# Kernel optimization log

Hardware: AMD Instinct MI355X
Metric: run time of the kernel (lower is better)

The kernel has to match this reference:

```python
import jax, jax.numpy as jnp
import numpy as np

B, S, E = 2, 2048, 1024
H = 16
D = E // H  # 64
SCALE = D ** -0.5


def setup_inputs() -> dict:
    key = jax.random.key(0)
    ks = jax.random.split(key, 9)
    w = lambda k: jax.random.normal(k, (E, E), dtype=jnp.float32) * 0.02
    b = lambda k: jax.random.normal(k, (E,), dtype=jnp.float32) * 0.02
    return {
        "hidden_states": jax.random.normal(ks[0], (B, S, E), dtype=jnp.float32),
        "q_w": w(ks[1]), "q_b": b(ks[2]),
        "k_w": w(ks[3]), "k_b": b(ks[4]),
        "v_w": w(ks[5]), "v_b": b(ks[6]),
        "o_w": w(ks[7]), "o_b": b(ks[8]),
    }


def reference(hidden_states, q_w, q_b, k_w, k_b, v_w, v_b, o_w, o_b):
    dtype = hidden_states.dtype
    # torch Linear: y = x @ W^T + b
    q = hidden_states @ q_w.T + q_b
    k = hidden_states @ k_w.T + k_b
    v = hidden_states @ v_w.T + v_b
    # [B,S,E] -> [B*H, S, D]
    split = lambda t: t.reshape(B, S, H, D).transpose(0, 2, 1, 3).reshape(B * H, S, D)
    q, k, v = split(q), split(k), split(v)
    # upcast_attention: fp32 QK^T, scaled (baddbmm with beta=0, no mask)
    scores = SCALE * jnp.einsum("bqd,bkd->bqk", q.astype(jnp.float32), k.astype(jnp.float32))
    # upcast_softmax: fp32 softmax over last dim (transpose_qk=False), cast back
    probs = jax.nn.softmax(scores, axis=-1).astype(dtype)
    # PV bmm, merge heads, out_proj (dropout p=0.0 -> identity)
    out = jnp.einsum("bqk,bkd->bqd", probs, v)
    out = out.reshape(B, H, S, D).transpose(0, 2, 1, 3).reshape(B, S, E)
    return out @ o_w.T + o_b
```

## Files before the change

kernel.cpp:

```cpp
#include <hip/hip_runtime.h>

typedef __bf16 bf16x8 __attribute__((ext_vector_type(8)));
typedef __bf16 bf16x4 __attribute__((ext_vector_type(4)));
typedef float  f32x4  __attribute__((ext_vector_type(4)));
typedef float  f32x16 __attribute__((ext_vector_type(16)));
typedef unsigned int u32x4 __attribute__((ext_vector_type(4)));

#define CS 0.18033688011112042f

__device__ __forceinline__ float fast_exp2(float x) {
    return __builtin_amdgcn_exp2f(x);
}

__device__ __forceinline__ f32x4 MFMA(bf16x8 a, bf16x8 b, f32x4 c) {
    return __builtin_amdgcn_mfma_f32_16x16x32_bf16(a, b, c, 0, 0, 0);
}
__device__ __forceinline__ f32x16 MFMA32(bf16x8 a, bf16x8 b, f32x16 c) {
    return __builtin_amdgcn_mfma_f32_32x32x16_bf16(a, b, c, 0, 0, 0);
}

__device__ __forceinline__ unsigned pk2(float a, float b) {
    union { __bf16 h[2]; unsigned u; } x;
    x.h[0] = (__bf16)a; x.h[1] = (__bf16)b;
    return x.u;
}

__device__ __forceinline__ void swap32(unsigned &a, unsigned &b) {
    asm volatile("v_permlane32_swap_b32 %0, %1" : "+v"(a), "+v"(b));
}

__global__ __launch_bounds__(256) void cvt5_kernel(
    const float* __restrict__ s0, const float* __restrict__ s1,
    const float* __restrict__ s2, const float* __restrict__ s3,
    const float* __restrict__ s4,
    __bf16* __restrict__ d0, __bf16* __restrict__ d1, __bf16* __restrict__ d2,
    __bf16* __restrict__ d3, __bf16* __restrict__ d4)
{
    int blk = blockIdx.x;
    const float* src; __bf16* dst; int base;
    if (blk < 4096)      { src = s0; dst = d0; base = blk; }
    else if (blk < 5120) { src = s1; dst = d1; base = blk - 4096; }
    else if (blk < 6144) { src = s2; dst = d2; base = blk - 5120; }
    else if (blk < 7168) { src = s3; dst = d3; base = blk - 6144; }
    else                 { src = s4; dst = d4; base = blk - 7168; }
    int i = base * 1024 + threadIdx.x * 4;
    float4 v = *(const float4*)(src + i);
    bf16x4 o;
    o[0] = (__bf16)v.x; o[1] = (__bf16)v.y; o[2] = (__bf16)v.z; o[3] = (__bf16)v.w;
    *(bf16x4*)(dst + i) = o;
}

template <typename OutT, int BN>
__device__ __forceinline__ void gemm_core(const __bf16* __restrict__ A,
                                          const __bf16* __restrict__ W,
                                          const float* __restrict__ bias,
                                          OutT* __restrict__ C,
                                          int m0, int n0, bool vtrans)
{
    constexpr int NJ = BN / 32;
    __shared__ __bf16 As[128 * 64];
    __shared__ __bf16 Bs[BN * 64];

    const int tid  = threadIdx.x;
    const int lane = tid & 63;
    const int w    = tid >> 6;
    const int wm   = w & 1;
    const int wn   = w >> 1;
    const int s    = lane & 15;
    const int q    = lane >> 4;

    f32x4 acc[4][NJ];
#pragma unroll
    for (int i = 0; i < 4; i++)
#pragma unroll
        for (int j = 0; j < NJ; j++)
#pragma unroll
            for (int r = 0; r < 4; r++) acc[i][j][r] = 0.0f;

    bf16x8 apre[4], bpre[NJ];
#pragma unroll
    for (int t = 0; t < 4; t++) {
        int c = tid + 256 * t, row = c >> 3, cc = c & 7;
        apre[t] = *(const bf16x8*)(A + (size_t)(m0 + row) * 1024 + cc * 8);
    }
#pragma unroll
    for (int t = 0; t < NJ; t++) {
        int c = tid + 256 * t, row = c >> 3, cc = c & 7;
        bpre[t] = *(const bf16x8*)(W + (size_t)(n0 + row) * 1024 + cc * 8);
    }

    for (int k0 = 0; k0 < 1024; k0 += 64) {
        __syncthreads();
#pragma unroll
        for (int t = 0; t < 4; t++) {
            int c = tid + 256 * t, row = c >> 3, cc = c & 7;
            *(bf16x8*)&As[row * 64 + ((cc ^ (row & 7)) << 3)] = apre[t];
        }
#pragma unroll
        for (int t = 0; t < NJ; t++) {
            int c = tid + 256 * t, row = c >> 3, cc = c & 7;
            *(bf16x8*)&Bs[row * 64 + ((cc ^ (row & 7)) << 3)] = bpre[t];
        }
        __syncthreads();

        if (k0 < 1024 - 64) {
            int kn = k0 + 64;
#pragma unroll
            for (int t = 0; t < 4; t++) {
                int c = tid + 256 * t, row = c >> 3, cc = c & 7;
                apre[t] = *(const bf16x8*)(A + (size_t)(m0 + row) * 1024 + kn + cc * 8);
            }
#pragma unroll
            for (int t = 0; t < NJ; t++) {
                int c = tid + 256 * t, row = c >> 3, cc = c & 7;
                bpre[t] = *(const bf16x8*)(W + (size_t)(n0 + row) * 1024 + kn + cc * 8);
            }
        }

#pragma unroll
        for (int kk = 0; kk < 2; kk++) {
            bf16x8 af[4], bf[NJ];
#pragma unroll
            for (int i = 0; i < 4; i++) {
                int row = wm * 64 + i * 16 + s;
                int idx = row * 64 + ((((kk << 2) + q) ^ (row & 7)) << 3);
                af[i] = *(const bf16x8*)&As[idx];
            }
#pragma unroll
            for (int j = 0; j < NJ; j++) {
                int row = wn * (BN / 2) + j * 16 + s;
                int idx = row * 64 + ((((kk << 2) + q) ^ (row & 7)) << 3);
                bf[j] = *(const bf16x8*)&Bs[idx];
            }
#pragma unroll
            for (int i = 0; i < 4; i++)
#pragma unroll
                for (int j = 0; j < NJ; j++)
                    acc[i][j] = MFMA(af[i], bf[j], acc[i][j]);
        }
    }

    if (vtrans) {
        __bf16* Vt = (__bf16*)C;
#pragma unroll
        for (int j = 0; j < NJ; j++) {
            int col = n0 + wn * (BN / 2) + j * 16 + s;
            int h   = col >> 6;
            int d   = col & 63;
            float bv = bias[col];
#pragma unroll
            for (int i = 0; i < 4; i++) {
                int rowb = m0 + wm * 64 + i * 16 + q * 4;
                int b    = rowb >> 11;
                int srow = rowb & 2047;
                bf16x4 pk;
#pragma unroll
                for (int r = 0; r < 4; r++) pk[r] = (__bf16)(acc[i][j][r] + bv);
                *(bf16x4*)&Vt[(size_t)((b * 16 + h) * 64 + d) * 2048 + srow] = pk;
            }
        }
    } else {
#pragma unroll
        for (int j = 0; j < NJ; j++) {
            int col = n0 + wn * (BN / 2) + j * 16 + s;
            float bv = bias[col];
#pragma unroll
            for (int i = 0; i < 4; i++) {
                int rowb = m0 + wm * 64 + i * 16 + q * 4;
#pragma unroll
                for (int r = 0; r < 4; r++) {
                    C[(size_t)(rowb + r) * 1024 + col] = (OutT)(acc[i][j][r] + bv);
                }
            }
        }
    }
}

__global__ __launch_bounds__(256) void gemm_qkv_kernel(
    const __bf16* __restrict__ X,
    const __bf16* __restrict__ Wq, const float* __restrict__ bq,
    const __bf16* __restrict__ Wk, const float* __restrict__ bk,
    const __bf16* __restrict__ Wv, const float* __restrict__ bv,
    __bf16* __restrict__ Q, __bf16* __restrict__ K, __bf16* __restrict__ Vt)
{
    int mt   = blockIdx.x & 31;
    int ntot = blockIdx.x >> 5;
    int which = ntot >> 3;
    const __bf16* W    = (which == 0) ? Wq : (which == 1) ? Wk : Wv;
    const float*  bias = (which == 0) ? bq : (which == 1) ? bk : bv;
    __bf16*       Out  = (which == 0) ? Q  : (which == 1) ? K  : Vt;
    gemm_core<__bf16, 128>(X, W, bias, Out, mt * 128, (ntot & 7) * 128, which == 2);
}

__global__ __launch_bounds__(256) void gemm_o_kernel(
    const __bf16* __restrict__ Ain, const __bf16* __restrict__ Wo,
    const float* __restrict__ bo, float* __restrict__ Out)
{
    int mt = blockIdx.x & 31;
    int nt = blockIdx.x >> 5;
    gemm_core<float, 64>(Ain, Wo, bo, Out, mt * 128, nt * 64, false);
}

__global__ __launch_bounds__(256, 2) void attn_kernel(
    const __bf16* __restrict__ Q, const __bf16* __restrict__ K,
    const __bf16* __restrict__ Vt, __bf16* __restrict__ O)
{
    __shared__ __bf16 k_lds[2][64 * 64];
    __shared__ __bf16 vt_lds[2][64 * 64];

    const int bh = blockIdx.x >> 4;
    const int qt = blockIdx.x & 15;
    const int b  = bh >> 4;
    const int h  = bh & 15;

    const int tid  = threadIdx.x;
    const int lane = tid & 63;
    const int w    = tid >> 6;
    const int qc   = lane & 31;
    const int hi   = lane >> 5;

    bf16x8 bq[4];
    {
        const int qrow = qt * 128 + w * 32 + qc;
        const __bf16* qp = Q + (size_t)(b * 2048 + qrow) * 1024 + h * 64 + hi * 8;
#pragma unroll
        for (int kd = 0; kd < 4; kd++)
            bq[kd] = *(const bf16x8*)(qp + kd * 16);
    }

    f32x16 acc[2];
#pragma unroll
    for (int nb = 0; nb < 2; nb++)
#pragma unroll
        for (int r = 0; r < 16; r++) acc[nb][r] = 0.0f;
    float lst = 0.0f;

    const __bf16* Kbase = K  + (size_t)b * 2048 * 1024 + h * 64;
    const __bf16* Vbase = Vt + (size_t)bh * 64 * 2048;

    bf16x8 kpre[2], vpre[2];
#pragma unroll
    for (int t = 0; t < 2; t++) {
        int c = tid + 256 * t;
        int krow = c >> 3, d16 = c & 7;
        kpre[t] = *(const bf16x8*)(Kbase + (size_t)krow * 1024 + d16 * 8);
        vpre[t] = *(const bf16x8*)(Vbase + (size_t)krow * 2048 + d16 * 8);
    }
#pragma unroll
    for (int t = 0; t < 2; t++) {
        int c = tid + 256 * t;
        int krow = c >> 3, d16 = c & 7;
        *(bf16x8*)&k_lds[0][krow * 64 + ((d16 ^ (krow & 7)) << 3)] = kpre[t];
        *(bf16x8*)&vt_lds[0][krow * 64 + ((d16 ^ (krow & 7)) << 3)] = vpre[t];
    }
#pragma unroll
    for (int t = 0; t < 2; t++) {
        int c = tid + 256 * t;
        int krow = c >> 3, d16 = c & 7;
        kpre[t] = *(const bf16x8*)(Kbase + (size_t)(64 + krow) * 1024 + d16 * 8);
        vpre[t] = *(const bf16x8*)(Vbase + (size_t)krow * 2048 + 64 + d16 * 8);
    }
    __syncthreads();

    int cur = 0;
    for (int kc = 0; kc < 32; kc++) {
        {
            __bf16* kwb = k_lds[cur ^ 1];
            __bf16* vwb = vt_lds[cur ^ 1];
#pragma unroll
            for (int t = 0; t < 2; t++) {
                int c = tid + 256 * t;
                int krow = c >> 3, d16 = c & 7;
                kwb[0] ? (void)0 : (void)0;
                *(bf16x8*)&kwb[krow * 64 + ((d16 ^ (krow & 7)) << 3)] = kpre[t];
                *(bf16x8*)&vwb[krow * 64 + ((d16 ^ (krow & 7)) << 3)] = vpre[t];
            }
        }
        {
            int kb2g = ((kc + 2) & 31) * 64;
#pragma unroll
            for (int t = 0; t < 2; t++) {
                int c = tid + 256 * t;
                int krow = c >> 3, d16 = c & 7;
                kpre[t] = *(const bf16x8*)(Kbase + (size_t)(kb2g + krow) * 1024 + d16 * 8);
                vpre[t] = *(const bf16x8*)(Vbase + (size_t)krow * 2048 + kb2g + d16 * 8);
            }
        }

        const __bf16* kbuf = k_lds[cur];
        const __bf16* vbuf = vt_lds[cur];

        f32x16 sc[2];
#pragma unroll
        for (int mb = 0; mb < 2; mb++)
#pragma unroll
            for (int r = 0; r < 16; r++) sc[mb][r] = 0.0f;
#pragma unroll
        for (int mb = 0; mb < 2; mb++) {
            int row = mb * 32 + qc;
            int rsw = row & 7;
#pragma unroll
            for (int kd = 0; kd < 4; kd++) {
                bf16x8 af = *(const bf16x8*)&kbuf[row * 64 + ((((kd << 1) | hi) ^ rsw) << 3)];
                sc[mb] = MFMA32(af, bq[kd], sc[mb]);
            }
        }

#pragma unroll
        for (int mb = 0; mb < 2; mb++) {
            float e[16];
            float rs = 0.0f;
#pragma unroll
            for (int r = 0; r < 16; r++) {
                e[r] = fast_exp2(sc[mb][r] * CS);
                rs += e[r];
            }
            lst += rs;
#pragma unroll
            for (int bb = 0; bb < 2; bb++) {
                unsigned w0 = pk2(e[8 * bb + 0], e[8 * bb + 1]);
                unsigned w1 = pk2(e[8 * bb + 2], e[8 * bb + 3]);
                unsigned w2 = pk2(e[8 * bb + 4], e[8 * bb + 5]);
                unsigned w3 = pk2(e[8 * bb + 6], e[8 * bb + 7]);
                swap32(w0, w2);
                swap32(w1, w3);
                u32x4 pw; pw[0] = w0; pw[1] = w1; pw[2] = w2; pw[3] = w3;
                bf16x8 pa = __builtin_bit_cast(bf16x8, pw);
                int kslot = ((mb << 1) | bb) << 1;
#pragma unroll
                for (int nb = 0; nb < 2; nb++) {
                    int d = nb * 32 + qc;
                    bf16x8 bv = *(const bf16x8*)&vbuf[d * 64 + (((kslot | hi) ^ (d & 7)) << 3)];
                    acc[nb] = MFMA32(pa, bv, acc[nb]);
                }
            }
        }
        __syncthreads();
        cur ^= 1;
    }

    float lt = lst + __shfl_xor(lst, 32);

    const size_t obase = (size_t)(b * 2048 + qt * 128 + w * 32) * 1024 + h * 64;
#pragma unroll
    for (int r = 0; r < 16; r++) {
        int row_rel = (r & 3) + 8 * (r >> 2) + 4 * hi;
        float lr = __shfl(lt, row_rel);
        float inv = 1.0f / lr;
#pragma unroll
        for (int nb = 0; nb < 2; nb++) {
            O[obase + (size_t)row_rel * 1024 + nb * 32 + qc] = (__bf16)(acc[nb][r] * inv);
        }
    }
}

extern "C" void kernel_launch(void* const* d_in, const int* in_sizes, int n_in,
                              void* d_out, int out_size, void* d_ws, size_t ws_size,
                              hipStream_t stream)
{
    const float* hs = (const float*)d_in[0];
    const float* qw = (const float*)d_in[1];
    const float* qb = (const float*)d_in[2];
    const float* kw = (const float*)d_in[3];
    const float* kb = (const float*)d_in[4];
    const float* vw = (const float*)d_in[5];
    const float* vb = (const float*)d_in[6];
    const float* ow = (const float*)d_in[7];
    const float* ob = (const float*)d_in[8];
    float* out = (float*)d_out;

    char* ws = (char*)d_ws;
    const size_t MB = (size_t)1024 * 1024;
    __bf16* Xb  = (__bf16*)(ws);
    __bf16* Wqb = (__bf16*)(ws +  8 * MB);
    __bf16* Wkb = (__bf16*)(ws + 10 * MB);
    __bf16* Wvb = (__bf16*)(ws + 12 * MB);
    __bf16* Wob = (__bf16*)(ws + 14 * MB);
    __bf16* Qb  = (__bf16*)(ws + 16 * MB);
    __bf16* Kb  = (__bf16*)(ws + 24 * MB);
    __bf16* Vtb = (__bf16*)(ws + 32 * MB);
    __bf16* Ab  = (__bf16*)(ws + 40 * MB);

    cvt5_kernel<<<dim3(8192), dim3(256), 0, stream>>>(hs, qw, kw, vw, ow,
                                                      Xb, Wqb, Wkb, Wvb, Wob);

    gemm_qkv_kernel<<<dim3(768), dim3(256), 0, stream>>>(Xb, Wqb, qb, Wkb, kb, Wvb, vb,
                                                         Qb, Kb, Vtb);
    attn_kernel<<<dim3(512), dim3(256), 0, stream>>>(Qb, Kb, Vtb, Ab);
    gemm_o_kernel<<<dim3(512), dim3(256), 0, stream>>>(Ab, Wob, ob, out);
}
```

Measured before the change: 187.9 us.

## Split attention KV range across two warp groups and fold softmax scale into Q

The attention kernel now runs 512 threads per block. Two groups of four waves each process half of the key/value sequence, and their partial accumulators and row sums are combined through LDS before normalisation. This doubles the waves available per query tile to improve latency hiding and CU occupancy, at the cost of extra LDS use and a reduction step. The softmax scale constant is also folded into the Q projection epilogue, which removes a multiply per score. That changes bf16 rounding of Q slightly.

```diff
diff --git a/kernel.cpp b/kernel.cpp
--- a/kernel.cpp
+++ b/kernel.cpp
@@ -55,7 +55,7 @@
                                           const __bf16* __restrict__ W,
                                           const float* __restrict__ bias,
                                           OutT* __restrict__ C,
-                                          int m0, int n0, bool vtrans)
+                                          int m0, int n0, bool vtrans, float oscale)
 {
     constexpr int NJ = BN / 32;
     __shared__ __bf16 As[128 * 64];
@@ -169,7 +169,7 @@
                 int rowb = m0 + wm * 64 + i * 16 + q * 4;
 #pragma unroll
                 for (int r = 0; r < 4; r++) {
-                    C[(size_t)(rowb + r) * 1024 + col] = (OutT)(acc[i][j][r] + bv);
+                    C[(size_t)(rowb + r) * 1024 + col] = (OutT)((acc[i][j][r] + bv) * oscale);
                 }
             }
         }
@@ -189,7 +189,8 @@
     const __bf16* W    = (which == 0) ? Wq : (which == 1) ? Wk : Wv;
     const float*  bias = (which == 0) ? bq : (which == 1) ? bk : bv;
     __bf16*       Out  = (which == 0) ? Q  : (which == 1) ? K  : Vt;
-    gemm_core<__bf16, 128>(X, W, bias, Out, mt * 128, (ntot & 7) * 128, which == 2);
+    float oscale = (which == 0) ? CS : 1.0f;
+    gemm_core<__bf16, 128>(X, W, bias, Out, mt * 128, (ntot & 7) * 128, which == 2, oscale);
 }
 
 __global__ __launch_bounds__(256) void gemm_o_kernel(
@@ -198,15 +199,14 @@
 {
     int mt = blockIdx.x & 31;
     int nt = blockIdx.x >> 5;
-    gemm_core<float, 64>(Ain, Wo, bo, Out, mt * 128, nt * 64, false);
-}
-
-__global__ __launch_bounds__(256, 2) void attn_kernel(
+    gemm_core<float, 64>(Ain, Wo, bo, Out, mt * 128, nt * 64, false, 1.0f);
+}
+
+__global__ __launch_bounds__(512, 4) void attn_kernel(
     const __bf16* __restrict__ Q, const __bf16* __restrict__ K,
     const __bf16* __restrict__ Vt, __bf16* __restrict__ O)
 {
-    __shared__ __bf16 k_lds[2][64 * 64];
-    __shared__ __bf16 vt_lds[2][64 * 64];
+    __shared__ __bf16 smem[2][2][2][64 * 64];
 
     const int bh = blockIdx.x >> 4;
     const int qt = blockIdx.x & 15;
@@ -216,12 +216,15 @@
     const int tid  = threadIdx.x;
     const int lane = tid & 63;
     const int w    = tid >> 6;
+    const int g    = w >> 2;
+    const int ws   = w & 3;
+    const int lt   = tid & 255;
     const int qc   = lane & 31;
     const int hi   = lane >> 5;
 
     bf16x8 bq[4];
     {
-        const int qrow = qt * 128 + w * 32 + qc;
+        const int qrow = qt * 128 + ws * 32 + qc;
         const __bf16* qp = Q + (size_t)(b * 2048 + qrow) * 1024 + h * 64 + hi * 8;
 #pragma unroll
         for (int kd = 0; kd < 4; kd++)
@@ -235,60 +238,59 @@
         for (int r = 0; r < 16; r++) acc[nb][r] = 0.0f;
     float lst = 0.0f;
 
-    const __bf16* Kbase = K  + (size_t)b * 2048 * 1024 + h * 64;
-    const __bf16* Vbase = Vt + (size_t)bh * 64 * 2048;
+    const __bf16* Kbase = K  + (size_t)(b * 2048 + g * 1024) * 1024 + h * 64;
+    const __bf16* Vbase = Vt + (size_t)bh * 64 * 2048 + g * 1024;
 
     bf16x8 kpre[2], vpre[2];
 #pragma unroll
     for (int t = 0; t < 2; t++) {
-        int c = tid + 256 * t;
-        int krow = c >> 3, d16 = c & 7;
-        kpre[t] = *(const bf16x8*)(Kbase + (size_t)krow * 1024 + d16 * 8);
-        vpre[t] = *(const bf16x8*)(Vbase + (size_t)krow * 2048 + d16 * 8);
+        int c = lt + 256 * t;
+        int krow = c >> 3, s16 = c & 7;
+        kpre[t] = *(const bf16x8*)(Kbase + (size_t)krow * 1024 + s16 * 8);
+        vpre[t] = *(const bf16x8*)(Vbase + (size_t)krow * 2048 + s16 * 8);
     }
 #pragma unroll
     for (int t = 0; t < 2; t++) {
-        int c = tid + 256 * t;
-        int krow = c >> 3, d16 = c & 7;
-        *(bf16x8*)&k_lds[0][krow * 64 + ((d16 ^ (krow & 7)) << 3)] = kpre[t];
-        *(bf16x8*)&vt_lds[0][krow * 64 + ((d16 ^ (krow & 7)) << 3)] = vpre[t];
+        int c = lt + 256 * t;
+        int krow = c >> 3, s16 = c & 7;
+        *(bf16x8*)&smem[g][0][0][krow * 64 + ((s16 ^ (krow & 7)) << 3)] = kpre[t];
+        *(bf16x8*)&smem[g][0][1][krow * 64 + ((s16 ^ (krow & 7)) << 3)] = vpre[t];
     }
 #pragma unroll
     for (int t = 0; t < 2; t++) {
-        int c = tid + 256 * t;
-        int krow = c >> 3, d16 = c & 7;
-        kpre[t] = *(const bf16x8*)(Kbase + (size_t)(64 + krow) * 1024 + d16 * 8);
-        vpre[t] = *(const bf16x8*)(Vbase + (size_t)krow * 2048 + 64 + d16 * 8);
+        int c = lt + 256 * t;
+        int krow = c >> 3, s16 = c & 7;
+        kpre[t] = *(const bf16x8*)(Kbase + (size_t)(64 + krow) * 1024 + s16 * 8);
+        vpre[t] = *(const bf16x8*)(Vbase + (size_t)krow * 2048 + 64 + s16 * 8);
     }
     __syncthreads();
 
     int cur = 0;
-    for (int kc = 0; kc < 32; kc++) {
+    for (int kc = 0; kc < 16; kc++) {
         {
-            __bf16* kwb = k_lds[cur ^ 1];
-            __bf16* vwb = vt_lds[cur ^ 1];
+            __bf16* kwb = smem[g][cur ^ 1][0];
+            __bf16* vwb = smem[g][cur ^ 1][1];
 #pragma unroll
             for (int t = 0; t < 2; t++) {
-                int c = tid + 256 * t;
-                int krow = c >> 3, d16 = c & 7;
-                kwb[0] ? (void)0 : (void)0;
-                *(bf16x8*)&kwb[krow * 64 + ((d16 ^ (krow & 7)) << 3)] = kpre[t];
-                *(bf16x8*)&vwb[krow * 64 + ((d16 ^ (krow & 7)) << 3)] = vpre[t];
+                int c = lt + 256 * t;
+                int krow = c >> 3, s16 = c & 7;
+                *(bf16x8*)&kwb[krow * 64 + ((s16 ^ (krow & 7)) << 3)] = kpre[t];
+                *(bf16x8*)&vwb[krow * 64 + ((s16 ^ (krow & 7)) << 3)] = vpre[t];
             }
         }
         {
-            int kb2g = ((kc + 2) & 31) * 64;
+            int kb2 = ((kc + 2) & 15) * 64;
 #pragma unroll
             for (int t = 0; t < 2; t++) {
-                int c = tid + 256 * t;
-                int krow = c >> 3, d16 = c & 7;
-                kpre[t] = *(const bf16x8*)(Kbase + (size_t)(kb2g + krow) * 1024 + d16 * 8);
-                vpre[t] = *(const bf16x8*)(Vbase + (size_t)krow * 2048 + kb2g + d16 * 8);
-            }
-        }
-
-        const __bf16* kbuf = k_lds[cur];
-        const __bf16* vbuf = vt_lds[cur];
+                int c = lt + 256 * t;
+                int krow = c >> 3, s16 = c & 7;
+                kpre[t] = *(const bf16x8*)(Kbase + (size_t)(kb2 + krow) * 1024 + s16 * 8);
+                vpre[t] = *(const bf16x8*)(Vbase + (size_t)krow * 2048 + kb2 + s16 * 8);
+            }
+        }
+
+        const __bf16* kbuf = smem[g][cur][0];
+        const __bf16* vbuf = smem[g][cur][1];
 
         f32x16 sc[2];
 #pragma unroll
@@ -309,13 +311,15 @@
 #pragma unroll
         for (int mb = 0; mb < 2; mb++) {
             float e[16];
-            float rs = 0.0f;
-#pragma unroll
-            for (int r = 0; r < 16; r++) {
-                e[r] = fast_exp2(sc[mb][r] * CS);
-                rs += e[r];
-            }
-            lst += rs;
+#pragma unroll
+            for (int r = 0; r < 16; r++)
+                e[r] = fast_exp2(sc[mb][r]);
+            float s0 = 0.f, s1 = 0.f, s2 = 0.f, s3 = 0.f;
+#pragma unroll
+            for (int r = 0; r < 16; r += 4) {
+                s0 += e[r]; s1 += e[r + 1]; s2 += e[r + 2]; s3 += e[r + 3];
+            }
+            lst += (s0 + s1) + (s2 + s3);
 #pragma unroll
             for (int bb = 0; bb < 2; bb++) {
                 unsigned w0 = pk2(e[8 * bb + 0], e[8 * bb + 1]);
@@ -339,17 +343,32 @@
         cur ^= 1;
     }
 
-    float lt = lst + __shfl_xor(lst, 32);
-
-    const size_t obase = (size_t)(b * 2048 + qt * 128 + w * 32) * 1024 + h * 64;
-#pragma unroll
-    for (int r = 0; r < 16; r++) {
-        int row_rel = (r & 3) + 8 * (r >> 2) + 4 * hi;
-        float lr = __shfl(lt, row_rel);
-        float inv = 1.0f / lr;
-#pragma unroll
-        for (int nb = 0; nb < 2; nb++) {
-            O[obase + (size_t)row_rel * 1024 + nb * 32 + qc] = (__bf16)(acc[nb][r] * inv);
+    float* cbuf = (float*)&smem[0][0][0][0];
+    if (g == 1) {
+        float* p = cbuf + ((size_t)ws * 64 + lane) * 36;
+        *(f32x16*)(p)      = acc[0];
+        *(f32x16*)(p + 16) = acc[1];
+        p[32] = lst;
+    }
+    __syncthreads();
+    if (g == 0) {
+        float* p = cbuf + ((size_t)ws * 64 + lane) * 36;
+        acc[0] += *(const f32x16*)(p);
+        acc[1] += *(const f32x16*)(p + 16);
+        lst += p[32];
+
+        float lt2 = lst + __shfl_xor(lst, 32);
+
+        const size_t obase = (size_t)(b * 2048 + qt * 128 + ws * 32) * 1024 + h * 64;
+#pragma unroll
+        for (int r = 0; r < 16; r++) {
+            int row_rel = (r & 3) + 8 * (r >> 2) + 4 * hi;
+            float lr = __shfl(lt2, row_rel);
+            float inv = 1.0f / lr;
+#pragma unroll
+            for (int nb = 0; nb < 2; nb++) {
+                O[obase + (size_t)row_rel * 1024 + nb * 32 + qc] = (__bf16)(acc[nb][r] * inv);
+            }
         }
     }
 }
@@ -386,6 +405,6 @@
 
     gemm_qkv_kernel<<<dim3(768), dim3(256), 0, stream>>>(Xb, Wqb, qb, Wkb, kb, Wvb, vb,
                                                          Qb, Kb, Vtb);
-    attn_kernel<<<dim3(512), dim3(256), 0, stream>>>(Qb, Kb, Vtb, Ab);
+    attn_kernel<<<dim3(512), dim3(512), 0, stream>>>(Qb, Kb, Vtb, Ab);
     gemm_o_kernel<<<dim3(512), dim3(256), 0, stream>>>(Ab, Wob, ob, out);
 }
```

Result: slower. 193.6 us (+3.0%).
